# Performance work log

Measured on AMD Instinct MI355X. Metric: run time of the kernel, lower is better.

## Reference

```python
import jax, jax.numpy as jnp
import numpy as np

B, SQ, SK = 2, 2048, 2048
DQ = DK = DV = DM = DOUT = 1024
H = 16
DHEAD = DM // H


def setup_inputs() -> dict:
    key = jax.random.key(0)
    ks = jax.random.split(key, 12)
    s = 0.02
    return {
        "Q": jax.random.normal(ks[0], (B, SQ, DQ), jnp.float32),
        "K": jax.random.normal(ks[1], (B, SK, DK), jnp.float32),
        "V": jax.random.normal(ks[2], (B, SK, DV), jnp.float32),
        "mask": jax.random.randint(ks[3], (B, 1, SK), 0, 2, jnp.int32),
        "Wq": jax.random.normal(ks[4], (DQ, DM), jnp.float32) * s,
        "bq": jnp.zeros((DM,), jnp.float32),
        "Wk": jax.random.normal(ks[5], (DK, DM), jnp.float32) * s,
        "bk": jnp.zeros((DM,), jnp.float32),
        "Wv": jax.random.normal(ks[6], (DV, DM), jnp.float32) * s,
        "bv": jnp.zeros((DM,), jnp.float32),
        "Wo": jax.random.normal(ks[7], (DM, DOUT), jnp.float32) * s,
        "bo": jnp.zeros((DOUT,), jnp.float32),
    }


def reference(Q, K, V, mask, Wq, bq, Wk, bk, Wv, bv, Wo, bo):
    b, sq, _ = Q.shape
    # QKV projections then split heads: (B, S, D) -> (B, H, S, d_k)
    q = (Q @ Wq + bq).reshape(b, sq, H, DHEAD).transpose(0, 2, 1, 3)
    k = (K @ Wk + bk).reshape(b, -1, H, DHEAD).transpose(0, 2, 1, 3)
    v = (V @ Wv + bv).reshape(b, -1, H, DHEAD).transpose(0, 2, 1, 3)
    # scores: (B, H, Sq, Sk)
    scores = jnp.einsum("bhqd,bhkd->bhqk", q, k) / np.sqrt(DHEAD).astype(np.float32)
    m = mask[:, None]  # (B,1,1,Sk), broadcast over heads and queries
    scores = jnp.where(m == 0, -jnp.inf, scores)
    attn = jax.nn.softmax(scores, axis=-1)
    out = jnp.einsum("bhqk,bhkd->bhqd", attn, v)
    out = out.transpose(0, 2, 1, 3).reshape(b, sq, DM)
    return out @ Wo + bo
```

## Files before the change

### kernel.cpp

```cpp
#include <hip/hip_runtime.h>
#include <hip/hip_bf16.h>

#define SQn 2048
#define SKn 2048
#define DMn 1024
#define NHn 16
#define DHn 64

typedef __attribute__((ext_vector_type(8))) short bf16x8;
typedef __attribute__((ext_vector_type(4))) float f32x4;

#define QSCALE 0.1803368801f

#define FBAR()                                     \
  __builtin_amdgcn_sched_barrier(0);               \
  asm volatile("s_barrier" ::: "memory");          \
  __builtin_amdgcn_sched_barrier(0)

__device__ __forceinline__ short f2bf(float f) {
  union { float f; unsigned u; } a; a.f = f;
  return (short)((a.u + 0x7FFFu + ((a.u >> 16) & 1u)) >> 16);
}

__device__ __forceinline__ unsigned cvt_pk_bf16(float lo, float hi) {
  unsigned r;
  asm("v_cvt_pk_bf16_f32 %0, %1, %2" : "=v"(r) : "v"(lo), "v"(hi));
  return r;
}

__device__ __forceinline__ void gload16(const void* g, void* l) {
  __builtin_amdgcn_global_load_lds(
      (__attribute__((address_space(1))) void*)g,
      (__attribute__((address_space(3))) void*)l, 16, 0, 0);
}

#define NCASTB 12288
__global__ __launch_bounds__(256) void prep(
    const float* __restrict__ Q, const float* __restrict__ K, const float* __restrict__ V,
    const float* __restrict__ W0, const float* __restrict__ W1,
    const float* __restrict__ W2, const float* __restrict__ W3,
    const int* __restrict__ mask,
    short* __restrict__ qkvOut, short* __restrict__ WtBase,
    int* __restrict__ pos, int* __restrict__ Lb) {
  const int blk = blockIdx.x;
  const int tid = threadIdx.x;
  __shared__ float t[32][33];
  __shared__ int part[256];
  __shared__ int base[256];

  if (blk < NCASTB) {
    const int n4each = (2 * 2048 * 1024) / 4;
    int i = blk * 256 + tid;
    const float* src;
    int j = i;
    if (i < n4each) src = Q;
    else if (i < 2 * n4each) { src = K; j = i - n4each; }
    else { src = V; j = i - 2 * n4each; }
    float4 f = ((const float4*)src)[j];
    short4 o;
    o.x = f2bf(f.x); o.y = f2bf(f.y); o.z = f2bf(f.z); o.w = f2bf(f.w);
    ((short4*)qkvOut)[i] = o;
  } else if (blk < NCASTB + 4096) {
    const int tt = blk - NCASTB;
    const int z = tt >> 10;
    const int rem = tt & 1023;
    const float* W = (z == 0) ? W0 : (z == 1) ? W1 : (z == 2) ? W2 : W3;
    short* Wt = WtBase + (size_t)z * DMn * DMn;
    const int bx = (rem & 31) * 32;
    const int by = (rem >> 5) * 32;
    const int tx = tid & 31, ty = tid >> 5;
#pragma unroll
    for (int j = 0; j < 4; ++j)
      t[ty + j * 8][tx] = W[(size_t)(by + ty + j * 8) * DMn + bx + tx];
    __syncthreads();
#pragma unroll
    for (int j = 0; j < 4; ++j)
      Wt[(size_t)(bx + ty + j * 8) * DMn + by + tx] = f2bf(t[tx][ty + j * 8]);
  } else {
    const int b = blk - NCASTB - 4096;
    const int* m = mask + b * SKn;
    int v[8];
    int s0 = 0;
#pragma unroll
    for (int j = 0; j < 8; ++j) { v[j] = m[tid * 8 + j] ? 1 : 0; s0 += v[j]; }
    part[tid] = s0;
    __syncthreads();
    if (tid == 0) {
      int acc = 0;
      for (int i = 0; i < 256; ++i) { base[i] = acc; acc += part[i]; }
      Lb[b] = acc;
    }
    __syncthreads();
    int acc = base[tid];
    int* p = pos + b * SKn;
#pragma unroll
    for (int j = 0; j < 8; ++j) { p[tid * 8 + j] = acc; acc += v[j]; }
  }
}

__global__ __launch_bounds__(512) void gemm_bt3(
    const short* __restrict__ A0, const short* __restrict__ A1, const short* __restrict__ A2,
    const short* __restrict__ B0, const short* __restrict__ B1, const short* __restrict__ B2,
    const float* __restrict__ c0, const float* __restrict__ c1, const float* __restrict__ c2,
    short* __restrict__ O0, short* __restrict__ O1, short* __restrict__ O2,
    const int* __restrict__ maskp, const int* __restrict__ posp,
    const int* __restrict__ Lp) {
  constexpr int K = 1024;
  const int z = blockIdx.z;
  const short* A  = (z == 0) ? A0 : (z == 1) ? A1 : A2;
  const short* Bt = (z == 0) ? B0 : (z == 1) ? B1 : B2;
  const float* bias = (z == 0) ? c0 : (z == 1) ? c1 : c2;
  short* Cout = (z == 0) ? O0 : (z == 1) ? O1 : O2;

  __shared__ short As[2][128 * 32];
  __shared__ short Bs[2][128 * 32];
  const int tid = threadIdx.x;
  const int lane = tid & 63;
  const int wid = tid >> 6;
  const int wr = wid >> 2, wc = wid & 3;
  const int bm = blockIdx.x * 128, bn = blockIdx.y * 128;

  f32x4 acc[4][2] = {};

  const int srow = tid >> 2;
  const int scol = (tid & 3) * 8;
  const short* Ag = A + (size_t)bm * K;
  const short* Bg = Bt + (size_t)bn * K;

#define GSTG(buf, k0)                                              \
  gload16(Ag + (size_t)srow * K + (k0) + scol, As[buf] + tid * 8); \
  gload16(Bg + (size_t)srow * K + (k0) + scol, Bs[buf] + tid * 8);

  GSTG(0, 0);
  GSTG(1, 32);

  const int rowA = wr * 64 + (lane & 15);
  const int rowB = wc * 32 + (lane & 15);
  const int ko = (lane >> 4) * 8;

  for (int t = 0; t < 32; ++t) {
    const int cur = t & 1;
    if (t < 31) asm volatile("s_waitcnt vmcnt(2)" ::: "memory");
    else        asm volatile("s_waitcnt vmcnt(0)" ::: "memory");
    FBAR();

    bf16x8 a[4], b[2];
#pragma unroll
    for (int m = 0; m < 4; ++m) a[m] = *(const bf16x8*)(As[cur] + (rowA + m * 16) * 32 + ko);
#pragma unroll
    for (int n = 0; n < 2; ++n) b[n] = *(const bf16x8*)(Bs[cur] + (rowB + n * 16) * 32 + ko);
    __builtin_amdgcn_s_setprio(1);
#pragma unroll
    for (int m = 0; m < 4; ++m)
#pragma unroll
      for (int n = 0; n < 2; ++n)
        acc[m][n] = __builtin_amdgcn_mfma_f32_16x16x32_bf16(a[m], b[n], acc[m][n], 0, 0, 0);
    __builtin_amdgcn_s_setprio(0);

    FBAR();
    if (t < 30) { GSTG(cur, t * 32 + 64); }
  }
#undef GSTG

  const int crow0 = bm + wr * 64 + ((lane >> 4) * 4);
  const int ccol0 = bn + wc * 32 + (lane & 15);
  float bv[2];
#pragma unroll
  for (int n = 0; n < 2; ++n) bv[n] = bias[ccol0 + n * 16];
#pragma unroll
  for (int m = 0; m < 4; ++m)
#pragma unroll
    for (int i = 0; i < 4; ++i) {
      int row = crow0 + m * 16 + i;
      int bb = row >> 11, s = row & 2047;
      if (z != 0) {
        int mm = maskp[(bb << 11) + s];
        int pp = posp[(bb << 11) + s];
        s = mm ? pp : (Lp[bb] + s - pp);
      }
#pragma unroll
      for (int n = 0; n < 2; ++n) {
        int col = ccol0 + n * 16;
        float val = acc[m][n][i] + bv[n];
        int hh = col >> 6, d = col & 63;
        if (z == 2) {
          Cout[((((size_t)bb * NHn + hh) * DHn + d) << 11) + s] = f2bf(val);
        } else {
          if (z == 0) val *= QSCALE;
          Cout[((((size_t)bb * NHn + hh) * SQn + s) << 6) + d] = f2bf(val);
        }
      }
    }
}

__global__ __launch_bounds__(256) void gemm_n64(const short* __restrict__ A,
                                                const short* __restrict__ Bt,
                                                const float* __restrict__ bias,
                                                float* __restrict__ C) {
  constexpr int K = 1024, N = 1024;
  __shared__ short As[2][128 * 32];
  __shared__ short Bs[2][64 * 32];
  const int tid = threadIdx.x;
  const int lane = tid & 63;
  const int wid = tid >> 6;
  const int wr = wid >> 1, wc = wid & 1;
  const int bm = blockIdx.x * 128, bn = blockIdx.y * 64;

  f32x4 acc[4][2] = {};

  const int srow = tid >> 2;
  const int scol = (tid & 3) * 8;
  const short* Ag = A + (size_t)bm * K;
  const short* Bg = Bt + (size_t)bn * K;

#define GSTG(buf, k0)                                                             \
  gload16(Ag + (size_t)srow * K + (k0) + scol,        As[buf] + tid * 8);         \
  gload16(Ag + (size_t)(srow + 64) * K + (k0) + scol, As[buf] + 2048 + tid * 8);  \
  gload16(Bg + (size_t)srow * K + (k0) + scol,        Bs[buf] + tid * 8);

  GSTG(0, 0);
  GSTG(1, 32);

  const int rowA = wr * 64 + (lane & 15);
  const int rowB = wc * 32 + (lane & 15);
  const int ko = (lane >> 4) * 8;

  for (int t = 0; t < 32; ++t) {
    const int cur = t & 1;
    if (t < 31) asm volatile("s_waitcnt vmcnt(3)" ::: "memory");
    else        asm volatile("s_waitcnt vmcnt(0)" ::: "memory");
    FBAR();

    bf16x8 a[4], b[2];
#pragma unroll
    for (int m = 0; m < 4; ++m) a[m] = *(const bf16x8*)(As[cur] + (rowA + m * 16) * 32 + ko);
#pragma unroll
    for (int n = 0; n < 2; ++n) b[n] = *(const bf16x8*)(Bs[cur] + (rowB + n * 16) * 32 + ko);
    __builtin_amdgcn_s_setprio(1);
#pragma unroll
    for (int m = 0; m < 4; ++m)
#pragma unroll
      for (int n = 0; n < 2; ++n)
        acc[m][n] = __builtin_amdgcn_mfma_f32_16x16x32_bf16(a[m], b[n], acc[m][n], 0, 0, 0);
    __builtin_amdgcn_s_setprio(0);

    FBAR();
    if (t < 30) { GSTG(cur, t * 32 + 64); }
  }
#undef GSTG

  const int crow0 = bm + wr * 64 + ((lane >> 4) * 4);
  const int ccol0 = bn + wc * 32 + (lane & 15);
#pragma unroll
  for (int m = 0; m < 4; ++m)
#pragma unroll
    for (int n = 0; n < 2; ++n) {
      int col = ccol0 + n * 16;
      float bv = bias[col];
#pragma unroll
      for (int i = 0; i < 4; ++i) {
        int row = crow0 + m * 16 + i;
        C[(size_t)row * N + col] = acc[m][n][i] + bv;
      }
    }
}

__global__ __launch_bounds__(512) void attn(const short* __restrict__ q,
                                            const short* __restrict__ k,
                                            const short* __restrict__ vt,
                                            const int* __restrict__ Lb,
                                            short* __restrict__ out) {
  __shared__ short Ks[2][64 * 64];
  __shared__ short Vs[2][64 * 64];
  __shared__ short Ps[8][16 * 64];

  const int tid = threadIdx.x;
  const int lane = tid & 63;
  const int w = tid >> 6;
  const int l = (blockIdx.x & 7) * 64 + (blockIdx.x >> 3);
  const int bh = l >> 4;
  const int qt = l & 15;
  const int h = bh & 15;
  const int b = bh >> 4;
  const size_t hoff = (size_t)bh * (SQn * DHn);

  const int c_ = lane & 15, g_ = lane >> 4;
  const int swz = (c_ & 7) << 4;

  const int L = Lb[b];
  const int nt = (L + 63) >> 6;
  const int lastt = nt - 1;

  bf16x8 qf[2];
  {
    const short* qp = q + hoff + (size_t)(qt * 128 + w * 16 + c_) * DHn + g_ * 8;
    qf[0] = *(const bf16x8*)qp;
    qf[1] = *(const bf16x8*)(qp + 32);
  }

  const int r0 = tid >> 3;
  const int gch = (tid & 7) ^ (r0 & 7);
  const size_t kO = (size_t)r0 * DHn + gch * 8;
  const size_t vO = (size_t)r0 * SKn + gch * 8;
  const int ldsO = tid * 8;

  float mrun = -1e30f;
  float lrun = 0.f;
  f32x4 o[4] = {};
  char* PwB = (char*)Ps[w];

#define STAGE(buf, kbase, vbase)            \
  gload16((kbase) + kO, &Ks[buf][ldsO]);    \
  gload16((vbase) + vO, &Vs[buf][ldsO]);

  const short* kpre = k + hoff;
  const short* vpre = vt + hoff;
  STAGE(0, kpre, vpre);
  kpre += 64 * DHn;
  vpre += 64;
  __syncthreads();

  int cur = 0;
  for (int kt = 0; kt < nt; ++kt) {
    if (kt + 1 < nt) {
      STAGE(cur ^ 1, kpre, vpre);
      kpre += 64 * DHn;
      vpre += 64;
    }

    const short* Kc = Ks[cur];
    const short* Vc = Vs[cur];

    f32x4 s[4];
    __builtin_amdgcn_s_setprio(1);
#pragma unroll
    for (int n = 0; n < 4; ++n) {
      f32x4 a = {};
      int key = n * 16 + c_;
#pragma unroll
      for (int kc = 0; kc < 2; ++kc) {
        int slot = (kc * 4 + g_) ^ (key & 7);
        bf16x8 kf = *(const bf16x8*)(Kc + key * 64 + slot * 8);
        a = __builtin_amdgcn_mfma_f32_16x16x32_bf16(kf, qf[kc], a, 0, 0, 0);
      }
      s[n] = a;
    }
    __builtin_amdgcn_s_setprio(0);

    if (kt == lastt) {
      const int kb = kt * 64 + g_ * 4;
#pragma unroll
      for (int n = 0; n < 4; ++n) {
        const int k0i = kb + n * 16;
        s[n][0] = (k0i + 0 < L) ? s[n][0] : -1e30f;
        s[n][1] = (k0i + 1 < L) ? s[n][1] : -1e30f;
        s[n][2] = (k0i + 2 < L) ? s[n][2] : -1e30f;
        s[n][3] = (k0i + 3 < L) ? s[n][3] : -1e30f;
      }
    }

    float pmax = fmaxf(fmaxf(s[0][0], s[0][1]), fmaxf(s[0][2], s[0][3]));
#pragma unroll
    for (int n = 1; n < 4; ++n)
      pmax = fmaxf(pmax, fmaxf(fmaxf(s[n][0], s[n][1]), fmaxf(s[n][2], s[n][3])));

    if (!__all(pmax - mrun <= 8.f)) {
      float pm = fmaxf(pmax, __shfl_xor(pmax, 16));
      pm = fmaxf(pm, __shfl_xor(pm, 32));
      float mn = fmaxf(mrun, pm);
      float sc = __builtin_amdgcn_exp2f(mrun - mn);
      mrun = mn;
      lrun *= sc;
      float scB[4];
#pragma unroll
      for (int i = 0; i < 4; ++i) scB[i] = __shfl(sc, g_ * 4 + i);
#pragma unroll
      for (int n = 0; n < 4; ++n)
#pragma unroll
        for (int i = 0; i < 4; ++i) o[n][i] *= scB[i];
    }

    float lsum = 0.f;
#pragma unroll
    for (int n = 0; n < 4; ++n) {
      float p0 = __builtin_amdgcn_exp2f(s[n][0] - mrun);
      float p1 = __builtin_amdgcn_exp2f(s[n][1] - mrun);
      float p2 = __builtin_amdgcn_exp2f(s[n][2] - mrun);
      float p3 = __builtin_amdgcn_exp2f(s[n][3] - mrun);
      lsum += (p0 + p1) + (p2 + p3);
      uint2 pk;
      pk.x = cvt_pk_bf16(p0, p1);
      pk.y = cvt_pk_bf16(p2, p3);
      *(uint2*)(PwB + ((c_ * 128) | ((n * 32 + g_ * 8) ^ swz))) = pk;
    }
    lrun += lsum;

    __builtin_amdgcn_s_setprio(1);
#pragma unroll
    for (int ks = 0; ks < 2; ++ks) {
      bf16x8 pf = *(const bf16x8*)(PwB + ((c_ * 128) | ((ks * 64 + g_ * 16) ^ swz)));
#pragma unroll
      for (int n = 0; n < 4; ++n) {
        int d = n * 16 + c_;
        int slot = (ks * 4 + g_) ^ (d & 7);
        bf16x8 vf = *(const bf16x8*)(Vc + d * 64 + slot * 8);
        o[n] = __builtin_amdgcn_mfma_f32_16x16x32_bf16(pf, vf, o[n], 0, 0, 0);
      }
    }
    __builtin_amdgcn_s_setprio(0);

    __syncthreads();
    cur ^= 1;
  }

  lrun += __shfl_xor(lrun, 16);
  lrun += __shfl_xor(lrun, 32);
  float lB[4];
#pragma unroll
  for (int i = 0; i < 4; ++i) lB[i] = __shfl(lrun, g_ * 4 + i);
#pragma unroll
  for (int n = 0; n < 4; ++n) {
#pragma unroll
    for (int i = 0; i < 4; ++i) {
      int srow = qt * 128 + w * 16 + g_ * 4 + i;
      int d = n * 16 + c_;
      out[((size_t)b * SQn + srow) * DMn + h * 64 + d] = f2bf(o[n][i] / lB[i]);
    }
  }
#undef STAGE
}

extern "C" void kernel_launch(void* const* d_in, const int* in_sizes, int n_in,
                              void* d_out, int out_size, void* d_ws, size_t ws_size,
                              hipStream_t stream) {
  const float* Q  = (const float*)d_in[0];
  const float* K  = (const float*)d_in[1];
  const float* V  = (const float*)d_in[2];
  const int* mask = (const int*)d_in[3];
  const float* Wq = (const float*)d_in[4];
  const float* bq = (const float*)d_in[5];
  const float* Wk = (const float*)d_in[6];
  const float* bk = (const float*)d_in[7];
  const float* Wv = (const float*)d_in[8];
  const float* bv = (const float*)d_in[9];
  const float* Wo = (const float*)d_in[10];
  const float* bo = (const float*)d_in[11];

  char* ws = (char*)d_ws;
  const size_t MB = 1024 * 1024;
  short* Qb  = (short*)(ws + 0 * MB);
  short* Wqt = (short*)(ws + 24 * MB);
  short* Wkt = (short*)(ws + 26 * MB);
  short* Wvt = (short*)(ws + 28 * MB);
  short* Wot = (short*)(ws + 30 * MB);
  short* qp  = (short*)(ws + 32 * MB);
  short* kp  = (short*)(ws + 40 * MB);
  short* vpt = (short*)(ws + 48 * MB);
  int*   posp = (int*)(ws + 56 * MB);
  int*   Lbp  = (int*)(ws + 56 * MB + 16384);
  short* Kb  = Qb + 4 * MB;
  short* Vb  = Qb + 8 * MB;
  short* ao  = Qb;

  prep<<<NCASTB + 4096 + 2, 256, 0, stream>>>(Q, K, V, Wq, Wk, Wv, Wo, mask,
                                              Qb, Wqt, posp, Lbp);

  gemm_bt3<<<dim3(32, 8, 3), 512, 0, stream>>>(Qb, Kb, Vb, Wqt, Wkt, Wvt,
                                               bq, bk, bv, qp, kp, vpt,
                                               mask, posp, Lbp);

  attn<<<512, 512, 0, stream>>>(qp, kp, vpt, Lbp, ao);

  gemm_n64<<<dim3(32, 16), 256, 0, stream>>>(ao, Wot, bo, (float*)d_out);
}
```

Baseline: 117.2 us.

## Gather unmasked K/V rows via inverse permutation and skip fully-masked GEMM tiles

```diff
diff --git a/kernel.cpp b/kernel.cpp
--- a/kernel.cpp
+++ b/kernel.cpp
@@ -41,12 +41,13 @@
     const float* __restrict__ W2, const float* __restrict__ W3,
     const int* __restrict__ mask,
     short* __restrict__ qkvOut, short* __restrict__ WtBase,
-    int* __restrict__ pos, int* __restrict__ Lb) {
+    int* __restrict__ inv, int* __restrict__ Lb) {
   const int blk = blockIdx.x;
   const int tid = threadIdx.x;
   __shared__ float t[32][33];
   __shared__ int part[256];
   __shared__ int base[256];
+  __shared__ int totL;
 
   if (blk < NCASTB) {
     const int n4each = (2 * 2048 * 1024) / 4;
@@ -89,12 +90,18 @@
       int acc = 0;
       for (int i = 0; i < 256; ++i) { base[i] = acc; acc += part[i]; }
       Lb[b] = acc;
+      totL = acc;
     }
     __syncthreads();
     int acc = base[tid];
-    int* p = pos + b * SKn;
-#pragma unroll
-    for (int j = 0; j < 8; ++j) { p[tid * 8 + j] = acc; acc += v[j]; }
+    int* ip = inv + b * SKn;
+#pragma unroll
+    for (int j = 0; j < 8; ++j) {
+      int s = tid * 8 + j;
+      int c = v[j] ? acc : (totL + s - acc);
+      ip[c] = s;
+      acc += v[j];
+    }
   }
 }
 
@@ -103,64 +110,54 @@
     const short* __restrict__ B0, const short* __restrict__ B1, const short* __restrict__ B2,
     const float* __restrict__ c0, const float* __restrict__ c1, const float* __restrict__ c2,
     short* __restrict__ O0, short* __restrict__ O1, short* __restrict__ O2,
-    const int* __restrict__ maskp, const int* __restrict__ posp,
-    const int* __restrict__ Lp) {
+    const int* __restrict__ invp, const int* __restrict__ Lp) {
   constexpr int K = 1024;
   const int z = blockIdx.z;
+  const int bm = blockIdx.x * 128, bn = blockIdx.y * 128;
+
+  if (z != 0 && (bm & 2047) >= Lp[bm >> 11]) return;
+
   const short* A  = (z == 0) ? A0 : (z == 1) ? A1 : A2;
   const short* Bt = (z == 0) ? B0 : (z == 1) ? B1 : B2;
   const float* bias = (z == 0) ? c0 : (z == 1) ? c1 : c2;
   short* Cout = (z == 0) ? O0 : (z == 1) ? O1 : O2;
 
-  __shared__ short As[2][128 * 32];
-  __shared__ short Bs[2][128 * 32];
+  __shared__ short As[128 * 32];
+  __shared__ short Bs[128 * 32];
   const int tid = threadIdx.x;
   const int lane = tid & 63;
   const int wid = tid >> 6;
   const int wr = wid >> 2, wc = wid & 3;
-  const int bm = blockIdx.x * 128, bn = blockIdx.y * 128;
 
   f32x4 acc[4][2] = {};
 
   const int srow = tid >> 2;
   const int scol = (tid & 3) * 8;
-  const short* Ag = A + (size_t)bm * K;
-  const short* Bg = Bt + (size_t)bn * K;
-
-#define GSTG(buf, k0)                                              \
-  gload16(Ag + (size_t)srow * K + (k0) + scol, As[buf] + tid * 8); \
-  gload16(Bg + (size_t)srow * K + (k0) + scol, Bs[buf] + tid * 8);
-
-  GSTG(0, 0);
-  GSTG(1, 32);
-
-  const int rowA = wr * 64 + (lane & 15);
-  const int rowB = wc * 32 + (lane & 15);
-  const int ko = (lane >> 4) * 8;
-
-  for (int t = 0; t < 32; ++t) {
-    const int cur = t & 1;
-    if (t < 31) asm volatile("s_waitcnt vmcnt(2)" ::: "memory");
-    else        asm volatile("s_waitcnt vmcnt(0)" ::: "memory");
-    FBAR();
+  int srcRow = bm + srow;
+  if (z != 0) srcRow = (srcRow & ~2047) | invp[srcRow];
+  const short* Arow = A + (size_t)srcRow * K;
+  const short* Brow = Bt + (size_t)(bn + srow) * K;
+
+  for (int k0 = 0; k0 < K; k0 += 32) {
+    __syncthreads();
+    gload16(Arow + k0 + scol, As + tid * 8);
+    gload16(Brow + k0 + scol, Bs + tid * 8);
+    __syncthreads();
 
     bf16x8 a[4], b[2];
-#pragma unroll
-    for (int m = 0; m < 4; ++m) a[m] = *(const bf16x8*)(As[cur] + (rowA + m * 16) * 32 + ko);
-#pragma unroll
-    for (int n = 0; n < 2; ++n) b[n] = *(const bf16x8*)(Bs[cur] + (rowB + n * 16) * 32 + ko);
-    __builtin_amdgcn_s_setprio(1);
+    const int rowA = wr * 64 + (lane & 15);
+    const int rowB = wc * 32 + (lane & 15);
+    const int ko = (lane >> 4) * 8;
+#pragma unroll
+    for (int m = 0; m < 4; ++m) a[m] = *(const bf16x8*)(As + (rowA + m * 16) * 32 + ko);
+#pragma unroll
+    for (int n = 0; n < 2; ++n) b[n] = *(const bf16x8*)(Bs + (rowB + n * 16) * 32 + ko);
 #pragma unroll
     for (int m = 0; m < 4; ++m)
 #pragma unroll
       for (int n = 0; n < 2; ++n)
         acc[m][n] = __builtin_amdgcn_mfma_f32_16x16x32_bf16(a[m], b[n], acc[m][n], 0, 0, 0);
-    __builtin_amdgcn_s_setprio(0);
-
-    FBAR();
-    if (t < 30) { GSTG(cur, t * 32 + 64); }
-  }
-#undef GSTG
+  }
 
   const int crow0 = bm + wr * 64 + ((lane >> 4) * 4);
   const int ccol0 = bn + wc * 32 + (lane & 15);
@@ -173,11 +170,6 @@
     for (int i = 0; i < 4; ++i) {
       int row = crow0 + m * 16 + i;
       int bb = row >> 11, s = row & 2047;
-      if (z != 0) {
-        int mm = maskp[(bb << 11) + s];
-        int pp = posp[(bb << 11) + s];
-        s = mm ? pp : (Lp[bb] + s - pp);
-      }
 #pragma unroll
       for (int n = 0; n < 2; ++n) {
         int col = ccol0 + n * 16;
@@ -456,18 +448,18 @@
   short* qp  = (short*)(ws + 32 * MB);
   short* kp  = (short*)(ws + 40 * MB);
   short* vpt = (short*)(ws + 48 * MB);
-  int*   posp = (int*)(ws + 56 * MB);
+  int*   invp = (int*)(ws + 56 * MB);
   int*   Lbp  = (int*)(ws + 56 * MB + 16384);
   short* Kb  = Qb + 4 * MB;
   short* Vb  = Qb + 8 * MB;
   short* ao  = Qb;
 
   prep<<<NCASTB + 4096 + 2, 256, 0, stream>>>(Q, K, V, Wq, Wk, Wv, Wo, mask,
-                                              Qb, Wqt, posp, Lbp);
+                                              Qb, Wqt, invp, Lbp);
 
   gemm_bt3<<<dim3(32, 8, 3), 512, 0, stream>>>(Qb, Kb, Vb, Wqt, Wkt, Wvt,
                                                bq, bk, bv, qp, kp, vpt,
-                                               mask, posp, Lbp);
+                                               invp, Lbp);
 
   attn<<<512, 512, 0, stream>>>(qp, kp, vpt, Lbp, ao);
 
```

After: 108.4 us, median of 2. -7.5%, faster.
